# Optimization experiments

Measured on AMD Instinct MI355X. Metric: run time of the kernel, lower is better.

Reference implementation:

```python
import jax, jax.numpy as jnp
import numpy as np

N = 50000
E = 600000
F_IN = 128
F_OUT = 128


def setup_inputs() -> dict:
    key = jax.random.key(0)
    k = jax.random.split(key, 8)
    x = jax.random.normal(k[0], (N, F_IN), dtype=jnp.float32)
    edge_index = jax.random.randint(k[1], (2, E), 0, N, dtype=jnp.int64)
    edge_weight = jax.random.uniform(k[2], (E,), dtype=jnp.float32)
    # glorot-initialized linear params (w1 is dead code in the original, kept for faithfulness)
    s = float(np.sqrt(6.0 / (F_IN + F_OUT)))
    W1 = jax.random.uniform(k[3], (F_IN, F_OUT), minval=-s, maxval=s, dtype=jnp.float32)
    b1 = jnp.zeros((F_OUT,), dtype=jnp.float32)
    W2 = jax.random.uniform(k[4], (F_IN, F_OUT), minval=-s, maxval=s, dtype=jnp.float32)
    b2 = jnp.zeros((F_OUT,), dtype=jnp.float32)
    a = jnp.full((1,), 0.5, dtype=jnp.float32)
    b = jnp.full((1,), 0.5, dtype=jnp.float32)
    return {"x": x, "edge_index": edge_index, "edge_weight": edge_weight,
            "W1": W1, "b1": b1, "W2": W2, "b2": b2, "a": a, "b": b}


def reference(x, edge_index, edge_weight, W1, b1, W2, b2, a, b):
    # wh_1 = self.w1(x)  (computed but unused in the original forward)
    wh_1 = x @ W1 + b1  # noqa: F841 (dead, DCE'd under jit)
    src, dst = edge_index[0], edge_index[1]
    # gather neighbor features [E, F_IN], scatter-sum to destination nodes [N, F_IN]
    x_j = jax.ops.segment_sum(x[src], dst, num_segments=N)
    wh_2 = x_j @ W2 + b2
    return wh_2
```

## Files before the change

kernel.cpp:

```cpp
#include <hip/hip_runtime.h>

#define F 128
#define CAP 64
#define LDT 136
#define TR 64
#define KC 32
#define LDA 36
#define LDW 160

typedef __attribute__((ext_vector_type(8))) short bf16x8;
typedef __attribute__((ext_vector_type(4))) float f32x4;

__device__ __forceinline__ unsigned short bf16r(float f)
{
    unsigned u = __float_as_uint(f);
    return (unsigned short)((u + 0x7fffu + ((u >> 16) & 1u)) >> 16);
}

__device__ __forceinline__ void load_edge(const int* __restrict__ ei, int is64,
                                          int E, int e, int& s, int& d)
{
    if (is64) {
        s = reinterpret_cast<const int2*>(ei)[e].x;
        d = reinterpret_cast<const int2*>(ei)[(size_t)E + e].x;
    } else {
        s = ei[e];
        d = ei[E + e];
    }
}

__global__ __launch_bounds__(256) void prep_kernel(
    const int* __restrict__ ei, const float* __restrict__ x,
    const float* __restrict__ W, int* __restrict__ flag,
    int* __restrict__ cursor, unsigned int* __restrict__ xh,
    unsigned short* __restrict__ Wt, int N, int M)
{
    int i = blockIdx.x * 256 + threadIdx.x;
    if (i < M) {
        float2 v = reinterpret_cast<const float2*>(x)[i];
        xh[i] = (unsigned)bf16r(v.x) | ((unsigned)bf16r(v.y) << 16);
    }
    if (i < N) cursor[i] = 0;
    if (i < F * F) {
        int k = i >> 7, n = i & 127;
        Wt[n * F + k] = bf16r(W[i]);
    }
    if (i == 0) {
        int or_hi = ei[1] | ei[3] | ei[5] | ei[7] | ei[9] | ei[11] | ei[13] | ei[15];
        *flag = (or_hi == 0) ? 1 : 0;
    }
}

__global__ __launch_bounds__(256) void position4_kernel(
    const int* __restrict__ ei, const int* __restrict__ flag_p,
    int* __restrict__ cursor, unsigned short* __restrict__ csr16, int E)
{
    const int tid = blockIdx.x * 256 + threadIdx.x;
    const int base = 4 * tid;
    if (base >= E) return;
    const int is64 = *flag_p;

    int s[4], d[4];
    int cnt;
    if (base + 3 < E && (E & 3) == 0) {
        cnt = 4;
        if (is64) {
            const int4* sp = reinterpret_cast<const int4*>(ei);
            int4 a = sp[tid * 2], b = sp[tid * 2 + 1];
            s[0] = a.x; s[1] = a.z; s[2] = b.x; s[3] = b.z;
            const int4* dp = reinterpret_cast<const int4*>(ei) + ((size_t)E >> 1);
            int4 c = dp[tid * 2], e4 = dp[tid * 2 + 1];
            d[0] = c.x; d[1] = c.z; d[2] = e4.x; d[3] = e4.z;
        } else {
            int4 sv = reinterpret_cast<const int4*>(ei)[tid];
            int4 dv = reinterpret_cast<const int4*>(ei + E)[tid];
            s[0] = sv.x; s[1] = sv.y; s[2] = sv.z; s[3] = sv.w;
            d[0] = dv.x; d[1] = dv.y; d[2] = dv.z; d[3] = dv.w;
        }
    } else {
        cnt = E - base; if (cnt > 4) cnt = 4;
        for (int j = 0; j < cnt; ++j) load_edge(ei, is64, E, base + j, s[j], d[j]);
        for (int j = cnt; j < 4; ++j) { s[j] = 0; d[j] = 0; }
    }

    int slot[4];
    #pragma unroll
    for (int j = 0; j < 4; ++j)
        slot[j] = (j < cnt) ? atomicAdd(&cursor[d[j]], 1) : CAP;
    #pragma unroll
    for (int j = 0; j < 4; ++j)
        if (slot[j] < CAP) csr16[(size_t)d[j] * CAP + slot[j]] = (unsigned short)s[j];
}

__device__ __forceinline__ float4 bf16x4_to_f4(uint2 u)
{
    float4 f;
    f.x = __uint_as_float(u.x << 16);
    f.y = __uint_as_float(u.x & 0xffff0000u);
    f.z = __uint_as_float(u.y << 16);
    f.w = __uint_as_float(u.y & 0xffff0000u);
    return f;
}

__global__ __launch_bounds__(256) void gather_bucket_kernel(
    const unsigned int* __restrict__ xh, const int* __restrict__ ei,
    const int* __restrict__ flag_p, const int* __restrict__ cursor,
    const unsigned short* __restrict__ csr16, unsigned int* __restrict__ aggbf,
    int N, int E)
{
    int node = blockIdx.x * 4 + (threadIdx.x >> 6);
    if (node >= N) return;
    int lane = threadIdx.x & 63;
    int half = lane >> 5;
    int col = lane & 31;
    int deg = cursor[node];

    const uint2* x2 = reinterpret_cast<const uint2*>(xh);
    float4 a0 = make_float4(0.f, 0.f, 0.f, 0.f);
    float4 a1 = make_float4(0.f, 0.f, 0.f, 0.f);

    if (deg <= CAP) {
        int sv = (lane < deg) ? (int)csr16[(size_t)node * CAP + lane] : 0;
        int i = 0;
        for (; i + 3 < deg; i += 4) {
            int e0 = __shfl(sv, i + half);
            int e1 = __shfl(sv, i + 2 + half);
            float4 v0 = bf16x4_to_f4(x2[(size_t)e0 * 32 + col]);
            float4 v1 = bf16x4_to_f4(x2[(size_t)e1 * 32 + col]);
            a0.x += v0.x; a0.y += v0.y; a0.z += v0.z; a0.w += v0.w;
            a1.x += v1.x; a1.y += v1.y; a1.z += v1.z; a1.w += v1.w;
        }
        for (; i + 1 < deg; i += 2) {
            int e0 = __shfl(sv, i + half);
            float4 v0 = bf16x4_to_f4(x2[(size_t)e0 * 32 + col]);
            a0.x += v0.x; a0.y += v0.y; a0.z += v0.z; a0.w += v0.w;
        }
        if (i < deg) {
            int e0 = __shfl(sv, i);
            if (half == 0) {
                float4 v = bf16x4_to_f4(x2[(size_t)e0 * 32 + col]);
                a0.x += v.x; a0.y += v.y; a0.z += v.z; a0.w += v.w;
            }
        }
    } else {
        int is64 = *flag_p;
        for (int base = 0; base < E; base += 64) {
            int e = base + lane;
            int s = 0, d = -1;
            if (e < E) load_edge(ei, is64, E, e, s, d);
            unsigned long long m = __ballot(d == node);
            while (m) {
                int i = __ffsll((long long)m) - 1;
                m &= m - 1;
                int sb = __shfl(s, i);
                float4 v = bf16x4_to_f4(x2[(size_t)sb * 32 + col]);
                if (half == 0) { a0.x += v.x; a0.y += v.y; a0.z += v.z; a0.w += v.w; }
            }
        }
    }
    a0.x += a1.x; a0.y += a1.y; a0.z += a1.z; a0.w += a1.w;
    a0.x += __shfl_xor(a0.x, 32);
    a0.y += __shfl_xor(a0.y, 32);
    a0.z += __shfl_xor(a0.z, 32);
    a0.w += __shfl_xor(a0.w, 32);
    if (half == 0) {
        uint2 o;
        o.x = (unsigned)bf16r(a0.x) | ((unsigned)bf16r(a0.y) << 16);
        o.y = (unsigned)bf16r(a0.z) | ((unsigned)bf16r(a0.w) << 16);
        reinterpret_cast<uint2*>(aggbf)[(size_t)node * 32 + col] = o;
    }
}

__global__ __launch_bounds__(256) void gemm_mfma_kernel(
    const unsigned short* __restrict__ aggbf, const unsigned short* __restrict__ Wt,
    const float* __restrict__ bias, float* __restrict__ out, int N)
{
    __shared__ unsigned short sWt[F * LDT];
    const int t = threadIdx.x;

    const uint4* Wg = reinterpret_cast<const uint4*>(Wt);
    #pragma unroll
    for (int u = 0; u < 8; ++u) {
        int idx = u * 256 + t;
        int n = idx >> 4;
        int c = idx & 15;
        *reinterpret_cast<uint4*>(&sWt[n * LDT + c * 8]) = Wg[idx];
    }
    __syncthreads();

    const int wv = t >> 6, lane = t & 63;
    const int quad = lane >> 4, n15 = lane & 15;
    const int rbase = blockIdx.x * 64 + wv * 16;

    f32x4 acc[8];
    #pragma unroll
    for (int i = 0; i < 8; ++i) acc[i] = (f32x4){0.f, 0.f, 0.f, 0.f};

    const int arow = rbase + n15;
    const bool aval = (arow < N);
    #pragma unroll
    for (int kc = 0; kc < F; kc += 32) {
        bf16x8 af;
        if (aval)
            af = *reinterpret_cast<const bf16x8*>(aggbf + (size_t)arow * F + kc + quad * 8);
        else
            af = (bf16x8){0, 0, 0, 0, 0, 0, 0, 0};
        #pragma unroll
        for (int nt = 0; nt < 8; ++nt) {
            bf16x8 bfr = *reinterpret_cast<const bf16x8*>(
                &sWt[(nt * 16 + n15) * LDT + kc + quad * 8]);
            acc[nt] = __builtin_amdgcn_mfma_f32_16x16x32_bf16(af, bfr, acc[nt], 0, 0, 0);
        }
    }

    #pragma unroll
    for (int nt = 0; nt < 8; ++nt) {
        float bv = bias[nt * 16 + n15];
        #pragma unroll
        for (int reg = 0; reg < 4; ++reg) {
            int row = rbase + quad * 4 + reg;
            if (row < N)
                out[(size_t)row * F + nt * 16 + n15] = acc[nt][reg] + bv;
        }
    }
}

__global__ __launch_bounds__(256) void init_kernel(
    const int* __restrict__ ei, int* __restrict__ flag,
    int* __restrict__ zero_arr, int N)
{
    int i = blockIdx.x * 256 + threadIdx.x;
    if (i < N) zero_arr[i] = 0;
    if (i == 0) {
        int or_hi = ei[1] | ei[3] | ei[5] | ei[7] | ei[9] | ei[11] | ei[13] | ei[15];
        *flag = (or_hi == 0) ? 1 : 0;
    }
}

__global__ __launch_bounds__(256) void position_bucket_kernel(
    const int* __restrict__ ei, const int* __restrict__ flag_p,
    int* __restrict__ cursor, int* __restrict__ csr_src, int E)
{
    int e = blockIdx.x * 256 + threadIdx.x;
    if (e >= E) return;
    int s, d;
    load_edge(ei, *flag_p, E, e, s, d);
    int slot = atomicAdd(&cursor[d], 1);
    if (slot < CAP) csr_src[(size_t)d * CAP + slot] = s;
}

__global__ __launch_bounds__(256) void gather_bucket_f32_kernel(
    const float* __restrict__ x, const int* __restrict__ ei,
    const int* __restrict__ flag_p, const int* __restrict__ cursor,
    const int* __restrict__ csr_src, float* __restrict__ agg, int N, int E)
{
    int node = blockIdx.x * 4 + (threadIdx.x >> 6);
    if (node >= N) return;
    int lane = threadIdx.x & 63;
    int half = lane >> 5;
    int col = lane & 31;
    int deg = cursor[node];

    const float4* x4 = reinterpret_cast<const float4*>(x);
    float4 a0 = make_float4(0.f, 0.f, 0.f, 0.f);
    float4 a1 = make_float4(0.f, 0.f, 0.f, 0.f);

    if (deg <= CAP) {
        int sv = (lane < deg) ? csr_src[(size_t)node * CAP + lane] : 0;
        int i = 0;
        for (; i + 3 < deg; i += 4) {
            int e0 = __shfl(sv, i + half);
            int e1 = __shfl(sv, i + 2 + half);
            float4 v0 = x4[(size_t)e0 * 32 + col];
            float4 v1 = x4[(size_t)e1 * 32 + col];
            a0.x += v0.x; a0.y += v0.y; a0.z += v0.z; a0.w += v0.w;
            a1.x += v1.x; a1.y += v1.y; a1.z += v1.z; a1.w += v1.w;
        }
        for (; i + 1 < deg; i += 2) {
            int e0 = __shfl(sv, i + half);
            float4 v0 = x4[(size_t)e0 * 32 + col];
            a0.x += v0.x; a0.y += v0.y; a0.z += v0.z; a0.w += v0.w;
        }
        if (i < deg) {
            int e0 = __shfl(sv, i);
            if (half == 0) {
                float4 v = x4[(size_t)e0 * 32 + col];
                a0.x += v.x; a0.y += v.y; a0.z += v.z; a0.w += v.w;
            }
        }
    } else {
        int is64 = *flag_p;
        for (int base = 0; base < E; base += 64) {
            int e = base + lane;
            int s = 0, d = -1;
            if (e < E) load_edge(ei, is64, E, e, s, d);
            unsigned long long m = __ballot(d == node);
            while (m) {
                int i = __ffsll((long long)m) - 1;
                m &= m - 1;
                int sb = __shfl(s, i);
                float4 v = x4[(size_t)sb * 32 + col];
                if (half == 0) { a0.x += v.x; a0.y += v.y; a0.z += v.z; a0.w += v.w; }
            }
        }
    }
    a0.x += a1.x; a0.y += a1.y; a0.z += a1.z; a0.w += a1.w;
    a0.x += __shfl_xor(a0.x, 32);
    a0.y += __shfl_xor(a0.y, 32);
    a0.z += __shfl_xor(a0.z, 32);
    a0.w += __shfl_xor(a0.w, 32);
    if (half == 0)
        reinterpret_cast<float4*>(agg)[(size_t)node * 32 + col] = a0;
}

__global__ __launch_bounds__(256) void scatter_kernel(
    const float* __restrict__ x, const int* __restrict__ ei,
    const int* __restrict__ flag_p, float* __restrict__ agg, int E)
{
    int tid = blockIdx.x * 256 + threadIdx.x;
    int e = tid >> 5;
    if (e >= E) return;
    int c = (tid & 31) << 2;
    int s, d;
    load_edge(ei, *flag_p, E, e, s, d);
    float4 v = *reinterpret_cast<const float4*>(x + (size_t)s * F + c);
    float* o = agg + (size_t)d * F + c;
    unsafeAtomicAdd(o + 0, v.x);
    unsafeAtomicAdd(o + 1, v.y);
    unsafeAtomicAdd(o + 2, v.z);
    unsafeAtomicAdd(o + 3, v.w);
}

__global__ __launch_bounds__(256) void gemm_kernel(
    float* __restrict__ io, const float* __restrict__ W,
    const float* __restrict__ bias, int N)
{
    __shared__ float sA[TR * LDA];
    __shared__ float sW[KC * LDW];
    const int t = threadIdx.x;
    const int row0 = blockIdx.x * TR;
    const int g = t & 7;
    const int r = t >> 3;

    float acc[2][16];
    #pragma unroll
    for (int i = 0; i < 2; ++i)
        #pragma unroll
        for (int j = 0; j < 16; ++j) acc[i][j] = 0.0f;

    for (int kc = 0; kc < F; kc += KC) {
        #pragma unroll
        for (int u = 0; u < 2; ++u) {
            int idx = u * 256 + t;
            int row = idx >> 3;
            int k4 = (idx & 7) * 4;
            int grow = row0 + row;
            float4 v = (grow < N)
                ? *reinterpret_cast<const float4*>(io + (size_t)grow * F + kc + k4)
                : make_float4(0.f, 0.f, 0.f, 0.f);
            *reinterpret_cast<float4*>(&sA[row * LDA + k4]) = v;
        }
        #pragma unroll
        for (int u = 0; u < 4; ++u) {
            int idx = u * 256 + t;
            int kk = idx >> 5;
            int f4 = (idx & 31) * 4;
            float4 v = *reinterpret_cast<const float4*>(W + (size_t)(kc + kk) * F + f4);
            int chunk = f4 >> 4;
            int within = f4 & 15;
            *reinterpret_cast<float4*>(&sW[kk * LDW + chunk * 20 + within]) = v;
        }
        __syncthreads();

        #pragma unroll 8
        for (int kk = 0; kk < KC; ++kk) {
            const float* wp = &sW[kk * LDW + g * 20];
            const float4 w0 = *reinterpret_cast<const float4*>(wp + 0);
            const float4 w1 = *reinterpret_cast<const float4*>(wp + 4);
            const float4 w2 = *reinterpret_cast<const float4*>(wp + 8);
            const float4 w3 = *reinterpret_cast<const float4*>(wp + 12);
            #pragma unroll
            for (int i = 0; i < 2; ++i) {
                const float xv = sA[(r * 2 + i) * LDA + kk];
                acc[i][0]  += xv * w0.x;  acc[i][1]  += xv * w0.y;
                acc[i][2]  += xv * w0.z;  acc[i][3]  += xv * w0.w;
                acc[i][4]  += xv * w1.x;  acc[i][5]  += xv * w1.y;
                acc[i][6]  += xv * w1.z;  acc[i][7]  += xv * w1.w;
                acc[i][8]  += xv * w2.x;  acc[i][9]  += xv * w2.y;
                acc[i][10] += xv * w2.z;  acc[i][11] += xv * w2.w;
                acc[i][12] += xv * w3.x;  acc[i][13] += xv * w3.y;
                acc[i][14] += xv * w3.z;  acc[i][15] += xv * w3.w;
            }
        }
        __syncthreads();
    }

    float bv[16];
    #pragma unroll
    for (int j = 0; j < 16; ++j) bv[j] = bias[g * 16 + j];
    #pragma unroll
    for (int i = 0; i < 2; ++i) {
        int row = row0 + r * 2 + i;
        if (row < N) {
            float* o = io + (size_t)row * F + g * 16;
            #pragma unroll
            for (int j4 = 0; j4 < 4; ++j4) {
                float4 v;
                v.x = acc[i][j4 * 4 + 0] + bv[j4 * 4 + 0];
                v.y = acc[i][j4 * 4 + 1] + bv[j4 * 4 + 1];
                v.z = acc[i][j4 * 4 + 2] + bv[j4 * 4 + 2];
                v.w = acc[i][j4 * 4 + 3] + bv[j4 * 4 + 3];
                *reinterpret_cast<float4*>(o + j4 * 4) = v;
            }
        }
    }
}

extern "C" void kernel_launch(void* const* d_in, const int* in_sizes, int n_in,
                              void* d_out, int out_size, void* d_ws, size_t ws_size,
                              hipStream_t stream) {
    const float* x  = (const float*)d_in[0];
    const int*   ei = (const int*)d_in[1];
    const float* W2 = (const float*)d_in[5];
    const float* b2 = (const float*)d_in[6];
    float* out = (float*)d_out;

    const int N = in_sizes[0] / F;
    const int E = in_sizes[2];
    const int nblk = (N + 255) / 256;
    const int M = N * (F / 2);
    const int eblk = (E + 255) / 256;

    int* ws = (int*)d_ws;
    size_t needA = (size_t)16 * 4 + (size_t)N * 4 + (size_t)N * CAP * 2
                 + (size_t)M * 4 + (size_t)F * F * 2 + (size_t)N * (F / 2) * 4;
    size_t needB = (size_t)(16 + N + (size_t)N * CAP) * sizeof(int);

    if (ws_size >= needA && N <= 65536) {
        int* flag    = ws;
        int* cursor  = flag + 16;
        unsigned short* csr16 = (unsigned short*)(cursor + N);
        unsigned int*   xh    = (unsigned int*)(csr16 + (size_t)N * CAP);
        unsigned short* Wt    = (unsigned short*)(xh + M);
        unsigned int*   aggbf = (unsigned int*)(Wt + F * F);

        int pmax = M; if (N > pmax) pmax = N; if (F * F > pmax) pmax = F * F;
        prep_kernel<<<(pmax + 255) / 256, 256, 0, stream>>>(
            ei, x, W2, flag, cursor, xh, Wt, N, M);
        int pblk = ((E + 3) / 4 + 255) / 256;
        position4_kernel<<<pblk, 256, 0, stream>>>(ei, flag, cursor, csr16, E);
        gather_bucket_kernel<<<(N + 3) / 4, 256, 0, stream>>>(
            xh, ei, flag, cursor, csr16, aggbf, N, E);
        gemm_mfma_kernel<<<(N + 63) / 64, 256, 0, stream>>>(
            (const unsigned short*)aggbf, Wt, b2, out, N);
    } else if (ws_size >= needB) {
        int* flag    = ws;
        int* cursor  = flag + 16;
        int* csr_src = cursor + N;
        init_kernel<<<nblk, 256, 0, stream>>>(ei, flag, cursor, N);
        position_bucket_kernel<<<eblk, 256, 0, stream>>>(ei, flag, cursor, csr_src, E);
        gather_bucket_f32_kernel<<<(N + 3) / 4, 256, 0, stream>>>(
            x, ei, flag, cursor, csr_src, out, N, E);
        gemm_kernel<<<(N + TR - 1) / TR, 256, 0, stream>>>(out, W2, b2, N);
    } else {
        int* flag = ws;
        init_kernel<<<1, 64, 0, stream>>>(ei, flag, flag + 16, 0);
        hipMemsetAsync(out, 0, (size_t)N * F * sizeof(float), stream);
        scatter_kernel<<<(E * 32 + 255) / 256, 256, 0, stream>>>(x, ei, flag, out, E);
        gemm_kernel<<<(N + TR - 1) / TR, 256, 0, stream>>>(out, W2, b2, N);
    }
}
```

Before: 161.4 us.

## Interleave degree counter with CSR slots and fuse bf16 conversion into positioning

Measured after the change: 167.1 us. 1.04x slower.

```diff
diff --git a/kernel.cpp b/kernel.cpp
--- a/kernel.cpp
+++ b/kernel.cpp
@@ -2,6 +2,7 @@
 
 #define F 128
 #define CAP 64
+#define RS 80
 #define LDT 136
 #define TR 64
 #define KC 32
@@ -29,67 +30,74 @@
     }
 }
 
-__global__ __launch_bounds__(256) void prep_kernel(
-    const int* __restrict__ ei, const float* __restrict__ x,
-    const float* __restrict__ W, int* __restrict__ flag,
-    int* __restrict__ cursor, unsigned int* __restrict__ xh,
-    unsigned short* __restrict__ Wt, int N, int M)
+__global__ __launch_bounds__(256) void zero_kernel(
+    const int* __restrict__ ei, int* __restrict__ flag,
+    uint4* __restrict__ rec4, int nrec4)
 {
     int i = blockIdx.x * 256 + threadIdx.x;
-    if (i < M) {
-        float2 v = reinterpret_cast<const float2*>(x)[i];
-        xh[i] = (unsigned)bf16r(v.x) | ((unsigned)bf16r(v.y) << 16);
-    }
-    if (i < N) cursor[i] = 0;
-    if (i < F * F) {
-        int k = i >> 7, n = i & 127;
-        Wt[n * F + k] = bf16r(W[i]);
-    }
+    int T = gridDim.x * 256;
+    for (int j = i; j < nrec4; j += T)
+        rec4[j] = make_uint4(0u, 0u, 0u, 0u);
     if (i == 0) {
         int or_hi = ei[1] | ei[3] | ei[5] | ei[7] | ei[9] | ei[11] | ei[13] | ei[15];
         *flag = (or_hi == 0) ? 1 : 0;
     }
 }
 
-__global__ __launch_bounds__(256) void position4_kernel(
-    const int* __restrict__ ei, const int* __restrict__ flag_p,
-    int* __restrict__ cursor, unsigned short* __restrict__ csr16, int E)
+__global__ __launch_bounds__(256) void posconv_kernel(
+    const int* __restrict__ ei, const float* __restrict__ x,
+    const float* __restrict__ W, const int* __restrict__ flag_p,
+    unsigned short* __restrict__ rec, unsigned int* __restrict__ xh,
+    unsigned short* __restrict__ Wt, int E, int M)
 {
     const int tid = blockIdx.x * 256 + threadIdx.x;
+    const int T = gridDim.x * 256;
+    const int is64 = *flag_p;
     const int base = 4 * tid;
-    if (base >= E) return;
-    const int is64 = *flag_p;
-
-    int s[4], d[4];
-    int cnt;
-    if (base + 3 < E && (E & 3) == 0) {
-        cnt = 4;
-        if (is64) {
-            const int4* sp = reinterpret_cast<const int4*>(ei);
-            int4 a = sp[tid * 2], b = sp[tid * 2 + 1];
-            s[0] = a.x; s[1] = a.z; s[2] = b.x; s[3] = b.z;
-            const int4* dp = reinterpret_cast<const int4*>(ei) + ((size_t)E >> 1);
-            int4 c = dp[tid * 2], e4 = dp[tid * 2 + 1];
-            d[0] = c.x; d[1] = c.z; d[2] = e4.x; d[3] = e4.z;
+
+    if (base < E) {
+        int s[4], d[4];
+        int cnt;
+        if (base + 3 < E && (E & 3) == 0) {
+            cnt = 4;
+            if (is64) {
+                const int4* sp = reinterpret_cast<const int4*>(ei);
+                int4 a = sp[tid * 2], b = sp[tid * 2 + 1];
+                s[0] = a.x; s[1] = a.z; s[2] = b.x; s[3] = b.z;
+                const int4* dp = reinterpret_cast<const int4*>(ei) + ((size_t)E >> 1);
+                int4 c = dp[tid * 2], e4 = dp[tid * 2 + 1];
+                d[0] = c.x; d[1] = c.z; d[2] = e4.x; d[3] = e4.z;
+            } else {
+                int4 sv = reinterpret_cast<const int4*>(ei)[tid];
+                int4 dv = reinterpret_cast<const int4*>(ei + E)[tid];
+                s[0] = sv.x; s[1] = sv.y; s[2] = sv.z; s[3] = sv.w;
+                d[0] = dv.x; d[1] = dv.y; d[2] = dv.z; d[3] = dv.w;
+            }
         } else {
-            int4 sv = reinterpret_cast<const int4*>(ei)[tid];
-            int4 dv = reinterpret_cast<const int4*>(ei + E)[tid];
-            s[0] = sv.x; s[1] = sv.y; s[2] = sv.z; s[3] = sv.w;
-            d[0] = dv.x; d[1] = dv.y; d[2] = dv.z; d[3] = dv.w;
-        }
-    } else {
-        cnt = E - base; if (cnt > 4) cnt = 4;
-        for (int j = 0; j < cnt; ++j) load_edge(ei, is64, E, base + j, s[j], d[j]);
-        for (int j = cnt; j < 4; ++j) { s[j] = 0; d[j] = 0; }
-    }
-
-    int slot[4];
-    #pragma unroll
-    for (int j = 0; j < 4; ++j)
-        slot[j] = (j < cnt) ? atomicAdd(&cursor[d[j]], 1) : CAP;
-    #pragma unroll
-    for (int j = 0; j < 4; ++j)
-        if (slot[j] < CAP) csr16[(size_t)d[j] * CAP + slot[j]] = (unsigned short)s[j];
+            cnt = E - base; if (cnt > 4) cnt = 4;
+            for (int j = 0; j < cnt; ++j) load_edge(ei, is64, E, base + j, s[j], d[j]);
+            for (int j = cnt; j < 4; ++j) { s[j] = 0; d[j] = 0; }
+        }
+        int slot[4];
+        #pragma unroll
+        for (int j = 0; j < 4; ++j)
+            slot[j] = (j < cnt)
+                ? atomicAdd(reinterpret_cast<int*>(rec + (size_t)d[j] * RS), 1) : CAP;
+        #pragma unroll
+        for (int j = 0; j < 4; ++j)
+            if (slot[j] < CAP)
+                rec[(size_t)d[j] * RS + 2 + slot[j]] = (unsigned short)s[j];
+    }
+
+    const float2* x2 = reinterpret_cast<const float2*>(x);
+    for (int j = tid; j < M; j += T) {
+        float2 v = x2[j];
+        xh[j] = (unsigned)bf16r(v.x) | ((unsigned)bf16r(v.y) << 16);
+    }
+    for (int j = tid; j < F * F; j += T) {
+        int k = j >> 7, n = j & 127;
+        Wt[n * F + k] = bf16r(W[j]);
+    }
 }
 
 __device__ __forceinline__ float4 bf16x4_to_f4(uint2 u)
@@ -104,23 +112,23 @@
 
 __global__ __launch_bounds__(256) void gather_bucket_kernel(
     const unsigned int* __restrict__ xh, const int* __restrict__ ei,
-    const int* __restrict__ flag_p, const int* __restrict__ cursor,
-    const unsigned short* __restrict__ csr16, unsigned int* __restrict__ aggbf,
-    int N, int E)
+    const int* __restrict__ flag_p, const unsigned short* __restrict__ rec,
+    unsigned int* __restrict__ aggbf, int N, int E)
 {
     int node = blockIdx.x * 4 + (threadIdx.x >> 6);
     if (node >= N) return;
     int lane = threadIdx.x & 63;
     int half = lane >> 5;
     int col = lane & 31;
-    int deg = cursor[node];
+    const unsigned short* r = rec + (size_t)node * RS;
+    int deg = *reinterpret_cast<const int*>(r);
 
     const uint2* x2 = reinterpret_cast<const uint2*>(xh);
     float4 a0 = make_float4(0.f, 0.f, 0.f, 0.f);
     float4 a1 = make_float4(0.f, 0.f, 0.f, 0.f);
 
     if (deg <= CAP) {
-        int sv = (lane < deg) ? (int)csr16[(size_t)node * CAP + lane] : 0;
+        int sv = (lane < deg) ? (int)r[2 + lane] : 0;
         int i = 0;
         for (; i + 3 < deg; i += 4) {
             int e0 = __shfl(sv, i + half);
@@ -432,25 +440,23 @@
     const int eblk = (E + 255) / 256;
 
     int* ws = (int*)d_ws;
-    size_t needA = (size_t)16 * 4 + (size_t)N * 4 + (size_t)N * CAP * 2
+    size_t needA = (size_t)16 * 4 + (size_t)N * RS * 2
                  + (size_t)M * 4 + (size_t)F * F * 2 + (size_t)N * (F / 2) * 4;
     size_t needB = (size_t)(16 + N + (size_t)N * CAP) * sizeof(int);
 
     if (ws_size >= needA && N <= 65536) {
-        int* flag    = ws;
-        int* cursor  = flag + 16;
-        unsigned short* csr16 = (unsigned short*)(cursor + N);
-        unsigned int*   xh    = (unsigned int*)(csr16 + (size_t)N * CAP);
-        unsigned short* Wt    = (unsigned short*)(xh + M);
+        int* flag = ws;
+        unsigned short* rec = (unsigned short*)(flag + 16);
+        unsigned int*   xh  = (unsigned int*)(rec + (size_t)N * RS);
+        unsigned short* Wt  = (unsigned short*)(xh + M);
         unsigned int*   aggbf = (unsigned int*)(Wt + F * F);
 
-        int pmax = M; if (N > pmax) pmax = N; if (F * F > pmax) pmax = F * F;
-        prep_kernel<<<(pmax + 255) / 256, 256, 0, stream>>>(
-            ei, x, W2, flag, cursor, xh, Wt, N, M);
+        int nrec4 = (int)(((size_t)N * RS * 2 + 15) / 16);
+        zero_kernel<<<256, 256, 0, stream>>>(ei, flag, (uint4*)rec, nrec4);
         int pblk = ((E + 3) / 4 + 255) / 256;
-        position4_kernel<<<pblk, 256, 0, stream>>>(ei, flag, cursor, csr16, E);
+        posconv_kernel<<<pblk, 256, 0, stream>>>(ei, x, W2, flag, rec, xh, Wt, E, M);
         gather_bucket_kernel<<<(N + 3) / 4, 256, 0, stream>>>(
-            xh, ei, flag, cursor, csr16, aggbf, N, E);
+            xh, ei, flag, rec, aggbf, N, E);
         gemm_mfma_kernel<<<(N + 63) / 64, 256, 0, stream>>>(
             (const unsigned short*)aggbf, Wt, b2, out, N);
     } else if (ws_size >= needB) {
```
